# Kernel optimization log

Hardware: AMD Instinct MI355X
Metric: run time of the kernel (lower is better)

## Reference

```python
import jax, jax.numpy as jnp
import numpy as np

H = 16      # numHeads (== numKeyValueHeads since keyValueHeadsPerHead=1)
D = 128     # headDim


def setup_inputs() -> dict:
    key = jax.random.key(0)
    k1, k2, k3 = jax.random.split(key, 3)
    B, S, dim = 2, 2048, 2048
    x = jax.random.normal(k1, (B, S, dim), dtype=jnp.float32)
    # qkvProj: Linear(dim -> (H + 2*H)*D) without bias; torch Linear weight is [out, in]
    Wqkv = jax.random.normal(k2, ((H + 2 * H) * D, dim), dtype=jnp.float32) * 0.02
    # outProj: Linear(H*D -> dim) without bias
    Wout = jax.random.normal(k3, (dim, H * D), dtype=jnp.float32) * 0.02
    return {"x": x, "Wqkv": Wqkv, "Wout": Wout}


def reference(x, Wqkv, Wout):
    B, S, _ = x.shape
    qkv = jnp.einsum('bsd,ed->bse', x, Wqkv)           # [B, S, 3*H*D]
    qkv = qkv.reshape(B, S, 3 * H, D)
    q = qkv[:, :, :H]                                  # [B, S, H, D]
    k = qkv[:, :, H:2 * H]                             # [B, S, H, D]
    v = qkv[:, :, 2 * H:]                              # [B, S, H, D]
    # explicit QK^T / sqrt(d), softmax in fp32, then @ V (keyValueHeadsPerHead=1
    # collapses the group axis, leaving standard per-head attention)
    logits = jnp.einsum('bqhd,bkhd->bhqk', q, k) * (D ** -0.5)
    w = jax.nn.softmax(logits.astype(jnp.float32), axis=-1).astype(logits.dtype)
    out = jnp.einsum('bhqk,bkhd->bqhd', w, v).reshape(B, S, H * D)
    return jnp.einsum('bse,de->bsd', out, Wout)        # outProj
```

## Files before the change

### kernel.cpp

```cpp
#include <hip/hip_runtime.h>

typedef __bf16 bf16x8 __attribute__((ext_vector_type(8)));
typedef _Float16 f16;
typedef f16 f16x8 __attribute__((ext_vector_type(8)));
typedef float f32x4 __attribute__((ext_vector_type(4)));
typedef unsigned short u16;
typedef u16 u16x4 __attribute__((ext_vector_type(4)));

__device__ __forceinline__ u16 f2bf(float f) {
  unsigned u = __builtin_bit_cast(unsigned, f);
  u += 0x7FFFu + ((u >> 16) & 1u);
  return (u16)(u >> 16);
}

#define GLDS16(g, l) __builtin_amdgcn_global_load_lds(                     \
    (const __attribute__((address_space(1))) unsigned int*)(g),            \
    (__attribute__((address_space(3))) unsigned int*)(l), 16, 0, 0)

__device__ __forceinline__ f32x4 mfma16(bf16x8 a, bf16x8 b, f32x4 c) {
  return __builtin_amdgcn_mfma_f32_16x16x32_bf16(a, b, c, 0, 0, 0);
}
__device__ __forceinline__ f32x4 mfma16h(f16x8 a, f16x8 b, f32x4 c) {
  return __builtin_amdgcn_mfma_f32_16x16x32_f16(a, b, c, 0, 0, 0);
}

__global__ void cvt_bf16(const float* __restrict__ src, u16* __restrict__ dst,
                         int n4, int n4s, float scale) {
  int idx = blockIdx.x * blockDim.x + threadIdx.x;
  int stride = gridDim.x * blockDim.x;
  for (int i = idx; i < n4; i += stride) {
    float4 v = ((const float4*)src)[i];
    float sc = (i < n4s) ? scale : 1.0f;
    u16x4 o = { f2bf(v.x * sc), f2bf(v.y * sc), f2bf(v.z * sc), f2bf(v.w * sc) };
    ((u16x4*)dst)[i] = o;
  }
}

template<int MODE>
__global__ __launch_bounds__(256, 2) void gemm_bt(
    const u16* __restrict__ A, const u16* __restrict__ B,
    void* __restrict__ C, u16* __restrict__ VT,
    int M, int N, int K) {
  __shared__ __align__(16) u16 As[128 * 32];
  __shared__ __align__(16) u16 Bs[128 * 32];
  const int t = threadIdx.x;
  const int lane = t & 63;
  const int w = t >> 6;
  const int wm = w >> 1, wn = w & 1;
  const int m0 = blockIdx.y * 128, n0 = blockIdx.x * 128;
  f32x4 acc[4][4] = {};

  const u16* ga = A + (size_t)(m0 + (t >> 2)) * K + (t & 3) * 8;
  const u16* gb = B + (size_t)(n0 + (t >> 2)) * K + (t & 3) * 8;
  u16* la = (u16*)As + t * 8;
  u16* lb = (u16*)Bs + t * 8;
  const size_t half = (size_t)64 * K;

  for (int k0 = 0; k0 < K; k0 += 32) {
    GLDS16(ga + k0, la);
    GLDS16(ga + half + k0, la + 2048);
    GLDS16(gb + k0, lb);
    GLDS16(gb + half + k0, lb + 2048);
    __syncthreads();
    const int ro = (lane & 15) * 32 + (lane >> 4) * 8;
    bf16x8 af[4], bfr[4];
#pragma unroll
    for (int i = 0; i < 4; ++i) af[i]  = *(const bf16x8*)&As[(wm * 64 + i * 16) * 32 + ro];
#pragma unroll
    for (int i = 0; i < 4; ++i) bfr[i] = *(const bf16x8*)&Bs[(wn * 64 + i * 16) * 32 + ro];
#pragma unroll
    for (int i = 0; i < 4; ++i)
#pragma unroll
      for (int j = 0; j < 4; ++j)
        acc[i][j] = mfma16(af[i], bfr[j], acc[i][j]);
    __syncthreads();
  }

  const int rbase = m0 + wm * 64 + ((lane >> 4) << 2);
  const int cbase = n0 + wn * 64 + (lane & 15);
#pragma unroll
  for (int i = 0; i < 4; ++i) {
#pragma unroll
    for (int j = 0; j < 4; ++j) {
      const int row0 = rbase + i * 16;
      const int col = cbase + j * 16;
      if (MODE == 0) {
        if (col < 4096) {
          u16* cq = (u16*)C;
#pragma unroll
          for (int jj = 0; jj < 4; ++jj)
            cq[(size_t)(row0 + jj) * 4096 + col] = f2bf(acc[i][j][jj]);
        } else {
          const int bb = row0 >> 11, s = row0 & 2047;
          auto h0 = __builtin_amdgcn_cvt_pkrtz(acc[i][j][0], acc[i][j][1]);
          auto h1 = __builtin_amdgcn_cvt_pkrtz(acc[i][j][2], acc[i][j][3]);
          uint2 pk;
          pk.x = __builtin_bit_cast(unsigned, h0);
          pk.y = __builtin_bit_cast(unsigned, h1);
          *(uint2*)&VT[(size_t)(bb * 2048 + (col - 4096)) * 2048 + s] = pk;
        }
      } else {
        float* cf = (float*)C;
#pragma unroll
        for (int jj = 0; jj < 4; ++jj)
          cf[(size_t)(row0 + jj) * N + col] = acc[i][j][jj];
      }
    }
  }
}

#define PSTRIDE 72
__global__ __launch_bounds__(512, 1) void attn_fwd(
    const u16* __restrict__ qk, const u16* __restrict__ vt, u16* __restrict__ aout) {
  __shared__ __align__(16) u16 Ks[2][64 * 128];
  __shared__ __align__(16) u16 Vs[2][128 * 64];
  __shared__ __align__(16) u16 Pl[8][32 * PSTRIDE];
  const int t = threadIdx.x, lane = t & 63, w = t >> 6;
  const int bh = blockIdx.x;
  const int b = bh >> 4, h = bh & 15;
  const int q0 = blockIdx.y * 256 + w * 32;
  const int l15 = lane & 15, lg = lane >> 4;

  const u16* qp = qk + (size_t)b * 2048 * 4096 + h * 128;
  const u16* kp = qp + 2048;
  const u16* vtp = vt + (size_t)(b * 16 + h) * 128 * 2048;
  u16* op = aout + (size_t)b * 2048 * 2048 + h * 128;

  int ksoff[2], vsoff[2];
#pragma unroll
  for (int rd = 0; rd < 2; ++rd) {
    const int r = rd * 32 + (t >> 4);
    const int c = (t & 15) ^ (r & 15);
    ksoff[rd] = r * 4096 + c * 8;
    const int rv = rd * 64 + (t >> 3);
    const int cv = (t & 7) ^ (rv & 7);
    vsoff[rd] = rv * 2048 + cv * 8;
  }

  bf16x8 qf[2][4];
#pragma unroll
  for (int mi = 0; mi < 2; ++mi)
#pragma unroll
    for (int kd = 0; kd < 4; ++kd)
      qf[mi][kd] = *(const bf16x8*)&qp[(size_t)(q0 + mi * 16 + l15) * 4096 + kd * 32 + lg * 8];

  f32x4 o[2][8] = {};
  f32x4 lacc[2] = {};
  const f16x8 onesf = {f16(1.f), f16(1.f), f16(1.f), f16(1.f),
                       f16(1.f), f16(1.f), f16(1.f), f16(1.f)};
  u16* pw = &Pl[w][0];

#pragma unroll
  for (int rd = 0; rd < 2; ++rd) {
    GLDS16(kp + ksoff[rd], &Ks[0][0] + rd * 4096 + t * 8);
    GLDS16(vtp + vsoff[rd], &Vs[0][0] + rd * 4096 + t * 8);
  }
  __syncthreads();

  auto tile = [&](const u16* ksb, const u16* vsb, u16* kpre, u16* vpre, int nextit) {
    if (nextit < 32) {
      const size_t kt1 = (size_t)nextit * 64;
#pragma unroll
      for (int rd = 0; rd < 2; ++rd) {
        GLDS16(kp + kt1 * 4096 + ksoff[rd], kpre + rd * 4096 + t * 8);
        GLDS16(vtp + kt1 + vsoff[rd], vpre + rd * 4096 + t * 8);
      }
    }
    f32x4 sf[2][4];
    __builtin_amdgcn_s_setprio(1);
#pragma unroll
    for (int ni = 0; ni < 4; ++ni) {
      const int r = ni * 16 + l15;
      bf16x8 kf[4];
#pragma unroll
      for (int kd = 0; kd < 4; ++kd)
        kf[kd] = *(const bf16x8*)&ksb[r * 128 + (((kd * 4 + lg) ^ l15) * 8)];
#pragma unroll
      for (int mi = 0; mi < 2; ++mi) {
        f32x4 s = {0.f, 0.f, 0.f, 0.f};
        s = mfma16(kf[0], qf[mi][0], s);
        s = mfma16(kf[1], qf[mi][1], s);
        s = mfma16(kf[2], qf[mi][2], s);
        s = mfma16(kf[3], qf[mi][3], s);
        sf[mi][ni] = s;
      }
    }
    __builtin_amdgcn_s_setprio(0);

#pragma unroll
    for (int mi = 0; mi < 2; ++mi)
#pragma unroll
      for (int ni = 0; ni < 4; ++ni) {
        float p0 = exp2f(sf[mi][ni][0]);
        float p1 = exp2f(sf[mi][ni][1]);
        float p2 = exp2f(sf[mi][ni][2]);
        float p3 = exp2f(sf[mi][ni][3]);
        auto h0 = __builtin_amdgcn_cvt_pkrtz(p0, p1);
        auto h1 = __builtin_amdgcn_cvt_pkrtz(p2, p3);
        uint2 wv;
        wv.x = __builtin_bit_cast(unsigned, h0);
        wv.y = __builtin_bit_cast(unsigned, h1);
        *(uint2*)&pw[(mi * 16 + l15) * PSTRIDE + ni * 16 + lg * 4] = wv;
      }

    f16x8 pa[2][2];
#pragma unroll
    for (int mi = 0; mi < 2; ++mi)
#pragma unroll
      for (int ks = 0; ks < 2; ++ks)
        pa[mi][ks] = *(const f16x8*)&pw[(mi * 16 + l15) * PSTRIDE + ks * 32 + lg * 8];
    __builtin_amdgcn_s_setprio(1);
#pragma unroll
    for (int mi = 0; mi < 2; ++mi) {
      lacc[mi] = mfma16h(pa[mi][0], onesf, lacc[mi]);
      lacc[mi] = mfma16h(pa[mi][1], onesf, lacc[mi]);
    }
#pragma unroll
    for (int n2 = 0; n2 < 8; ++n2) {
      const int r = n2 * 16 + l15;
      f16x8 vf0 = *(const f16x8*)&vsb[r * 64 + (((0 * 4 + lg) ^ (l15 & 7)) * 8)];
      f16x8 vf1 = *(const f16x8*)&vsb[r * 64 + (((1 * 4 + lg) ^ (l15 & 7)) * 8)];
#pragma unroll
      for (int mi = 0; mi < 2; ++mi) {
        o[mi][n2] = mfma16h(pa[mi][0], vf0, o[mi][n2]);
        o[mi][n2] = mfma16h(pa[mi][1], vf1, o[mi][n2]);
      }
    }
    __builtin_amdgcn_s_setprio(0);
    __syncthreads();
  };

#pragma unroll 1
  for (int it = 0; it < 32; it += 2) {
    tile(&Ks[0][0], &Vs[0][0], &Ks[1][0], &Vs[1][0], it + 1);
    tile(&Ks[1][0], &Vs[1][0], &Ks[0][0], &Vs[0][0], it + 2);
  }

#pragma unroll
  for (int mi = 0; mi < 2; ++mi)
#pragma unroll
    for (int j = 0; j < 4; ++j) {
      float inv = 1.f / lacc[mi][j];
#pragma unroll
      for (int n2 = 0; n2 < 8; ++n2)
        op[(size_t)(q0 + mi * 16 + lg * 4 + j) * 2048 + n2 * 16 + l15] =
            f2bf(o[mi][n2][j] * inv);
    }
}

extern "C" void kernel_launch(void* const* d_in, const int* in_sizes, int n_in,
                              void* d_out, int out_size, void* d_ws, size_t ws_size,
                              hipStream_t stream) {
  const float* x    = (const float*)d_in[0];
  const float* Wqkv = (const float*)d_in[1];
  const float* Wout = (const float*)d_in[2];
  float* out = (float*)d_out;

  u16* ws = (u16*)d_ws;
  u16* xb    = ws;
  u16* wqkvb = ws + 8388608;
  u16* woutb = ws + 20971520;
  u16* qkbuf = ws + 25165824;
  u16* vtbuf = ws + 41943040;
  u16* aout  = xb;

  const float qscale = 0.08838834764831845f * 1.4426950408889634f;

  cvt_bf16<<<2048, 256, 0, stream>>>(x,    xb,    8388608 / 4, 0, 1.0f);
  cvt_bf16<<<2048, 256, 0, stream>>>(Wqkv, wqkvb, 12582912 / 4, 4194304 / 4, qscale);
  cvt_bf16<<<1024, 256, 0, stream>>>(Wout, woutb, 4194304 / 4, 0, 1.0f);

  gemm_bt<0><<<dim3(48, 32), 256, 0, stream>>>(xb, wqkvb, (void*)qkbuf, vtbuf,
                                               4096, 6144, 2048);
  attn_fwd<<<dim3(32, 8, 1), 512, 0, stream>>>(qkbuf, vtbuf, aout);
  gemm_bt<1><<<dim3(16, 32), 256, 0, stream>>>(aout, woutb, (void*)out, nullptr,
                                               4096, 2048, 2048);
}
```

Before: 278.5 us.

## Add dedicated QKV GEMM kernel with 256x256 tiles and 4-stage LDS pipeline

Replaces the generic 128x128 single-buffered QKV projection GEMM with a dedicated 512-thread kernel. The new kernel uses 256x256 tiles, a 4-deep global-to-LDS prefetch ring with explicit vmcnt waits, an XOR-swizzled LDS layout to avoid bank conflicts, and a grouped block-index remap for L2 locality. The goal is to hide global load latency and raise MFMA utilisation in the largest GEMM. In exchange it uses 128 KB of LDS and many accumulator registers, so occupancy and register pressure are risks. The output projection keeps the old kernel, now simplified to fp32 output only.

```diff
diff --git a/kernel.cpp b/kernel.cpp
--- a/kernel.cpp
+++ b/kernel.cpp
@@ -36,11 +36,109 @@
   }
 }
 
-template<int MODE>
+__global__ __launch_bounds__(512, 2) void gemm1_qkv(
+    const u16* __restrict__ A, const u16* __restrict__ B,
+    u16* __restrict__ QK, u16* __restrict__ VT) {
+  __shared__ __align__(16) u16 L[4][16384];
+  constexpr int K = 2048;
+  const int t = threadIdx.x, lane = t & 63, w = t >> 6;
+  const int wm = w >> 2, wn = w & 3;
+  const int l15 = lane & 15, lg = lane >> 4;
+
+  const int bid = blockIdx.x;
+  const int wg = (bid & 7) * 48 + (bid >> 3);
+  const int bx = wg % 24, by = wg / 24;
+  const int m0 = by * 256, n0 = bx * 256;
+
+  const int csrc = ((t & 3) ^ ((t >> 2) & 3) ^ ((t >> 4) & 3)) * 8;
+  const u16* ga = A + (size_t)(m0 + (t >> 2)) * K + csrc;
+  const u16* gb = B + (size_t)(n0 + (t >> 2)) * K + csrc;
+  const int rchunk = (lg ^ (l15 & 3) ^ (l15 >> 2)) * 8;
+
+  f32x4 acc[8][4] = {};
+
+#define STAGE1(kt, bf) do {                                                \
+    u16* la_ = &L[bf][0]; u16* lb_ = &L[bf][8192];                         \
+    const int ko_ = (kt) * 32;                                             \
+    GLDS16(ga + ko_,           la_ + t * 8);                               \
+    GLDS16(ga + ko_ + 128 * K, la_ + 4096 + t * 8);                        \
+    GLDS16(gb + ko_,           lb_ + t * 8);                               \
+    GLDS16(gb + ko_ + 128 * K, lb_ + 4096 + t * 8);                        \
+  } while (0)
+
+#define GBODY(kt, VM) do {                                                 \
+    asm volatile("s_waitcnt vmcnt(" #VM ")" ::: "memory");                 \
+    __builtin_amdgcn_sched_barrier(0);                                     \
+    __builtin_amdgcn_s_barrier();                                          \
+    __builtin_amdgcn_sched_barrier(0);                                     \
+    const u16* la_ = &L[(kt) & 3][0];                                      \
+    const u16* lb_ = &L[(kt) & 3][8192];                                   \
+    bf16x8 af[8]; bf16x8 bfr[4];                                           \
+    _Pragma("unroll")                                                      \
+    for (int i_ = 0; i_ < 8; ++i_)                                         \
+      af[i_] = *(const bf16x8*)&la_[(wm * 128 + i_ * 16 + l15) * 32 + rchunk]; \
+    _Pragma("unroll")                                                      \
+    for (int j_ = 0; j_ < 4; ++j_)                                         \
+      bfr[j_] = *(const bf16x8*)&lb_[(wn * 64 + j_ * 16 + l15) * 32 + rchunk]; \
+    __builtin_amdgcn_s_setprio(1);                                         \
+    _Pragma("unroll")                                                      \
+    for (int i_ = 0; i_ < 8; ++i_)                                         \
+      _Pragma("unroll")                                                    \
+      for (int j_ = 0; j_ < 4; ++j_)                                       \
+        acc[i_][j_] = mfma16(af[i_], bfr[j_], acc[i_][j_]);                \
+    __builtin_amdgcn_s_setprio(0);                                         \
+    asm volatile("s_waitcnt lgkmcnt(0)" ::: "memory");                     \
+    __builtin_amdgcn_sched_barrier(0);                                     \
+    __builtin_amdgcn_s_barrier();                                          \
+    __builtin_amdgcn_sched_barrier(0);                                     \
+  } while (0)
+
+  STAGE1(0, 0); STAGE1(1, 1); STAGE1(2, 2);
+#pragma unroll 1
+  for (int it = 0; it <= 60; ++it) {
+    STAGE1(it + 3, (it + 3) & 3);
+    GBODY(it, 12);
+  }
+  GBODY(61, 8);
+  GBODY(62, 4);
+  GBODY(63, 0);
+#undef STAGE1
+#undef GBODY
+
+  const int rb = m0 + wm * 128 + lg * 4;
+  const int cb0 = wn * 64 + l15;
+  if (n0 < 4096) {
+#pragma unroll
+    for (int i = 0; i < 8; ++i)
+#pragma unroll
+      for (int j = 0; j < 4; ++j) {
+        const int row0 = rb + i * 16;
+        const int col = n0 + cb0 + j * 16;
+#pragma unroll
+        for (int jj = 0; jj < 4; ++jj)
+          QK[(size_t)(row0 + jj) * 4096 + col] = f2bf(acc[i][j][jj]);
+      }
+  } else {
+#pragma unroll
+    for (int i = 0; i < 8; ++i)
+#pragma unroll
+      for (int j = 0; j < 4; ++j) {
+        const int row0 = rb + i * 16;
+        const int vcol = (n0 - 4096) + cb0 + j * 16;
+        const int bb = row0 >> 11, s = row0 & 2047;
+        auto h0 = __builtin_amdgcn_cvt_pkrtz(acc[i][j][0], acc[i][j][1]);
+        auto h1 = __builtin_amdgcn_cvt_pkrtz(acc[i][j][2], acc[i][j][3]);
+        uint2 pk;
+        pk.x = __builtin_bit_cast(unsigned, h0);
+        pk.y = __builtin_bit_cast(unsigned, h1);
+        *(uint2*)&VT[((size_t)bb * 2048 + vcol) * 2048 + s] = pk;
+      }
+  }
+}
+
 __global__ __launch_bounds__(256, 2) void gemm_bt(
     const u16* __restrict__ A, const u16* __restrict__ B,
-    void* __restrict__ C, u16* __restrict__ VT,
-    int M, int N, int K) {
+    float* __restrict__ C, int M, int N, int K) {
   __shared__ __align__(16) u16 As[128 * 32];
   __shared__ __align__(16) u16 Bs[128 * 32];
   const int t = threadIdx.x;
@@ -79,34 +177,15 @@
   const int rbase = m0 + wm * 64 + ((lane >> 4) << 2);
   const int cbase = n0 + wn * 64 + (lane & 15);
 #pragma unroll
-  for (int i = 0; i < 4; ++i) {
+  for (int i = 0; i < 4; ++i)
 #pragma unroll
     for (int j = 0; j < 4; ++j) {
       const int row0 = rbase + i * 16;
       const int col = cbase + j * 16;
-      if (MODE == 0) {
-        if (col < 4096) {
-          u16* cq = (u16*)C;
-#pragma unroll
-          for (int jj = 0; jj < 4; ++jj)
-            cq[(size_t)(row0 + jj) * 4096 + col] = f2bf(acc[i][j][jj]);
-        } else {
-          const int bb = row0 >> 11, s = row0 & 2047;
-          auto h0 = __builtin_amdgcn_cvt_pkrtz(acc[i][j][0], acc[i][j][1]);
-          auto h1 = __builtin_amdgcn_cvt_pkrtz(acc[i][j][2], acc[i][j][3]);
-          uint2 pk;
-          pk.x = __builtin_bit_cast(unsigned, h0);
-          pk.y = __builtin_bit_cast(unsigned, h1);
-          *(uint2*)&VT[(size_t)(bb * 2048 + (col - 4096)) * 2048 + s] = pk;
-        }
-      } else {
-        float* cf = (float*)C;
-#pragma unroll
-        for (int jj = 0; jj < 4; ++jj)
-          cf[(size_t)(row0 + jj) * N + col] = acc[i][j][jj];
-      }
-    }
-  }
+#pragma unroll
+      for (int jj = 0; jj < 4; ++jj)
+        C[(size_t)(row0 + jj) * N + col] = acc[i][j][jj];
+    }
 }
 
 #define PSTRIDE 72
@@ -270,9 +349,7 @@
   cvt_bf16<<<2048, 256, 0, stream>>>(Wqkv, wqkvb, 12582912 / 4, 4194304 / 4, qscale);
   cvt_bf16<<<1024, 256, 0, stream>>>(Wout, woutb, 4194304 / 4, 0, 1.0f);
 
-  gemm_bt<0><<<dim3(48, 32), 256, 0, stream>>>(xb, wqkvb, (void*)qkbuf, vtbuf,
-                                               4096, 6144, 2048);
+  gemm1_qkv<<<384, 512, 0, stream>>>(xb, wqkvb, qkbuf, vtbuf);
   attn_fwd<<<dim3(32, 8, 1), 512, 0, stream>>>(qkbuf, vtbuf, aout);
-  gemm_bt<1><<<dim3(16, 32), 256, 0, stream>>>(aout, woutb, (void*)out, nullptr,
-                                               4096, 2048, 2048);
-}
+  gemm_bt<<<dim3(16, 32), 256, 0, stream>>>(aout, woutb, out, 4096, 2048, 2048);
+}
```

Result: slower. 286.2 us (+2.8%).

## Double-buffer GEMM LDS tiles with prefetch, XOR swizzle, and raised occupancy

Applied to the files above, without the earlier changes.

The projection GEMM kernel now keeps two LDS buffers and issues the global-to-LDS loads for the next K tile before computing on the current one, using explicit waitcnt and barriers so the load latency overlaps the MFMA work. The LDS layout is XOR-swizzled by row to reduce bank conflicts on the fragment reads. It also raises the launch-bounds occupancy hint and raises wave priority around the MFMA block. LDS use per block doubles, which may limit occupancy, and the hand-placed waitcnt and barriers are fragile.

```diff
diff --git a/kernel.cpp b/kernel.cpp
--- a/kernel.cpp
+++ b/kernel.cpp
@@ -37,47 +37,79 @@
 }
 
 template<int MODE>
-__global__ __launch_bounds__(256, 2) void gemm_bt(
+__global__ __launch_bounds__(256, 3) void gemm_bt(
     const u16* __restrict__ A, const u16* __restrict__ B,
     void* __restrict__ C, u16* __restrict__ VT,
     int M, int N, int K) {
-  __shared__ __align__(16) u16 As[128 * 32];
-  __shared__ __align__(16) u16 Bs[128 * 32];
+  __shared__ __align__(16) u16 As[2][128 * 32];
+  __shared__ __align__(16) u16 Bs[2][128 * 32];
   const int t = threadIdx.x;
   const int lane = t & 63;
   const int w = t >> 6;
   const int wm = w >> 1, wn = w & 1;
+  const int l15 = lane & 15, lg = lane >> 4;
   const int m0 = blockIdx.y * 128, n0 = blockIdx.x * 128;
   f32x4 acc[4][4] = {};
 
-  const u16* ga = A + (size_t)(m0 + (t >> 2)) * K + (t & 3) * 8;
-  const u16* gb = B + (size_t)(n0 + (t >> 2)) * K + (t & 3) * 8;
-  u16* la = (u16*)As + t * 8;
-  u16* lb = (u16*)Bs + t * 8;
+  const int srow = t >> 2;
+  const int schunk = (t & 3) ^ ((srow >> 1) & 3);
+  const u16* ga = A + (size_t)(m0 + srow) * K + schunk * 8;
+  const u16* gb = B + (size_t)(n0 + srow) * K + schunk * 8;
   const size_t half = (size_t)64 * K;
-
-  for (int k0 = 0; k0 < K; k0 += 32) {
-    GLDS16(ga + k0, la);
-    GLDS16(ga + half + k0, la + 2048);
-    GLDS16(gb + k0, lb);
-    GLDS16(gb + half + k0, lb + 2048);
-    __syncthreads();
-    const int ro = (lane & 15) * 32 + (lane >> 4) * 8;
-    bf16x8 af[4], bfr[4];
-#pragma unroll
-    for (int i = 0; i < 4; ++i) af[i]  = *(const bf16x8*)&As[(wm * 64 + i * 16) * 32 + ro];
-#pragma unroll
-    for (int i = 0; i < 4; ++i) bfr[i] = *(const bf16x8*)&Bs[(wn * 64 + i * 16) * 32 + ro];
-#pragma unroll
-    for (int i = 0; i < 4; ++i)
-#pragma unroll
-      for (int j = 0; j < 4; ++j)
-        acc[i][j] = mfma16(af[i], bfr[j], acc[i][j]);
-    __syncthreads();
-  }
-
-  const int rbase = m0 + wm * 64 + ((lane >> 4) << 2);
-  const int cbase = n0 + wn * 64 + (lane & 15);
+  const int ro = l15 * 32 + ((lg ^ ((l15 >> 1) & 3)) * 8);
+
+#define STG(kt, bf) do {                                                   \
+    const int ko_ = (kt) * 32;                                             \
+    GLDS16(ga + ko_,        &As[bf][0] + t * 8);                           \
+    GLDS16(ga + half + ko_, &As[bf][2048] + t * 8);                        \
+    GLDS16(gb + ko_,        &Bs[bf][0] + t * 8);                           \
+    GLDS16(gb + half + ko_, &Bs[bf][2048] + t * 8);                        \
+  } while (0)
+
+#define BODY(bf) do {                                                      \
+    const u16* la_ = &As[bf][0];                                           \
+    const u16* lb_ = &Bs[bf][0];                                           \
+    bf16x8 af[4], bfr[4];                                                  \
+    _Pragma("unroll")                                                      \
+    for (int i_ = 0; i_ < 4; ++i_)                                         \
+      af[i_] = *(const bf16x8*)&la_[(wm * 64 + i_ * 16) * 32 + ro];        \
+    _Pragma("unroll")                                                      \
+    for (int i_ = 0; i_ < 4; ++i_)                                         \
+      bfr[i_] = *(const bf16x8*)&lb_[(wn * 64 + i_ * 16) * 32 + ro];       \
+    __builtin_amdgcn_s_setprio(1);                                         \
+    _Pragma("unroll")                                                      \
+    for (int i_ = 0; i_ < 4; ++i_)                                         \
+      _Pragma("unroll")                                                    \
+      for (int j_ = 0; j_ < 4; ++j_)                                       \
+        acc[i_][j_] = mfma16(af[i_], bfr[j_], acc[i_][j_]);                \
+    __builtin_amdgcn_s_setprio(0);                                         \
+  } while (0)
+
+  const int NT = K / 32;
+  STG(0, 0);
+#pragma unroll 1
+  for (int T = 0; T < NT - 1; ++T) {
+    STG(T + 1, (T + 1) & 1);
+    asm volatile("s_waitcnt vmcnt(4)" ::: "memory");
+    __builtin_amdgcn_sched_barrier(0);
+    __builtin_amdgcn_s_barrier();
+    __builtin_amdgcn_sched_barrier(0);
+    BODY(T & 1);
+    asm volatile("s_waitcnt lgkmcnt(0)" ::: "memory");
+    __builtin_amdgcn_sched_barrier(0);
+    __builtin_amdgcn_s_barrier();
+    __builtin_amdgcn_sched_barrier(0);
+  }
+  asm volatile("s_waitcnt vmcnt(0)" ::: "memory");
+  __builtin_amdgcn_sched_barrier(0);
+  __builtin_amdgcn_s_barrier();
+  __builtin_amdgcn_sched_barrier(0);
+  BODY((NT - 1) & 1);
+#undef STG
+#undef BODY
+
+  const int rbase = m0 + wm * 64 + (lg << 2);
+  const int cbase = n0 + wn * 64 + l15;
 #pragma unroll
   for (int i = 0; i < 4; ++i) {
 #pragma unroll
```

Result: no change. 277.0 us (-0.5%).
